# Performance work log

Measured on AMD Instinct MI355X. Metric: run time of the kernel, lower is better.

The kernel has to match this reference:

```python
import jax, jax.numpy as jnp
import numpy as np

B, T, D, K = 64, 512, 1024, 10
TEMP = 0.07
EPS = 1e-8


def setup_inputs() -> dict:
    key = jax.random.key(0)
    features = jax.random.normal(key, (B, T, D), dtype=jnp.float32)
    # Replicate torch.randperm-based negative sampling: for each batch b,
    # sample K indices without replacement from the (B-1)*T vectors of all
    # other batches, then map flat index -> (batch, time).
    rng = np.random.default_rng(0)
    neg_b = np.empty((B, K), dtype=np.int64)
    neg_t = np.empty((B, K), dtype=np.int64)
    for b in range(B):
        idx = rng.permutation((B - 1) * T)[:K]
        bb = idx // T
        bb = bb + (bb >= b)  # skip own batch
        neg_b[b] = bb
        neg_t[b] = idx % T
    return {"features": features, "neg_b": jnp.asarray(neg_b), "neg_t": jnp.asarray(neg_t)}


def _unit(x):
    # torch F.cosine_similarity semantics: divide by max(||x||, eps)
    n = jnp.sqrt(jnp.sum(x * x, axis=-1, keepdims=True))
    return x / jnp.maximum(n, EPS)


def reference(features, neg_b, neg_t):
    anchors = features[:, 1:T - 1, :]     # [B, T-2, D]
    positives = features[:, 2:T, :]       # [B, T-2, D]
    a_hat = _unit(anchors)
    pos_sim = jnp.sum(a_hat * _unit(positives), axis=-1) / TEMP          # [B, T-2]
    negs = jax.lax.stop_gradient(features)[neg_b, neg_t]                  # [B, K, D]
    sim_neg = jnp.einsum('btd,bkd->btk', a_hat, _unit(negs)) / TEMP       # [B, T-2, K]
    exp_pos = jnp.exp(pos_sim)
    exp_neg = jnp.exp(sim_neg).sum(axis=-1)
    loss = -jnp.log(exp_pos / (exp_pos + exp_neg))                        # [B, T-2]
    return loss.mean(axis=1).mean()
```

## Files before the change

kernel.cpp:

```cpp
#include <hip/hip_runtime.h>

typedef unsigned int uint;
typedef _Float16 f16x2 __attribute__((ext_vector_type(2)));

#define B_ 64
#define T_ 512
#define K_ 10
constexpr float TEMP_ = 0.07f;
constexpr float EPS_ = 1e-8f;
constexpr int F4ROW = 256;
constexpr int APW = 8;
constexpr int NBLK = 16;
constexpr int ROWU = 512;

__device__ __forceinline__ float dot4(float4 a, float4 b) {
    return a.x * b.x + a.y * b.y + a.z * b.z + a.w * b.w;
}
__device__ __forceinline__ f16x2 bc_(uint u){ return __builtin_bit_cast(f16x2, u); }
__device__ __forceinline__ f16x2 pkrtz(float a, float b){
    return __builtin_bit_cast(f16x2, __builtin_amdgcn_cvt_pkrtz(a, b));
}
__device__ __forceinline__ uint pkrtz_u(float a, float b){
    return __builtin_bit_cast(uint, __builtin_amdgcn_cvt_pkrtz(a, b));
}

template <int CTRL>
__device__ __forceinline__ float dpp_add(float x){
    int y = __builtin_amdgcn_update_dpp(0, __float_as_int(x), CTRL, 0xf, 0xf, false);
    return x + __int_as_float(y);
}
__device__ __forceinline__ float red6(float x){
    x = dpp_add<0x128>(x);
    x = dpp_add<0x124>(x);
    x = dpp_add<0x122>(x);
    x = dpp_add<0x121>(x);
    x = dpp_add<0x142>(x);
    x = dpp_add<0x143>(x);
    return x;
}
__device__ __forceinline__ float red64(float x){
    x = red6(x);
    return __shfl(x, 63, 64);
}

__global__ __launch_bounds__(64) void signcl_prep(
    const float* __restrict__ features,
    const int* __restrict__ neg_b,
    const int* __restrict__ neg_t,
    uint* __restrict__ negs_pk)
{
    const int blk = blockIdx.x;
    const int b = blk / K_, k = blk % K_;
    const int l = threadIdx.x;

    const int nb = neg_b[b * K_ + k];
    const int nt = neg_t[b * K_ + k];
    const float4* rp = reinterpret_cast<const float4*>(features)
                       + ((size_t)nb * T_ + nt) * F4ROW + l * 4;
    float4 v0 = rp[0], v1 = rp[1], v2 = rp[2], v3 = rp[3];
    float ss = dot4(v0, v0) + dot4(v1, v1) + dot4(v2, v2) + dot4(v3, v3);
    ss = red64(ss);
    const float inv = 1.f / fmaxf(sqrtf(ss), EPS_);

    uint4* out = reinterpret_cast<uint4*>(negs_pk + ((size_t)b * K_ + k) * ROWU);
    uint4 o;
    o.x = pkrtz_u(v0.x * inv, v0.y * inv);
    o.y = pkrtz_u(v0.z * inv, v0.w * inv);
    o.z = pkrtz_u(v1.x * inv, v1.y * inv);
    o.w = pkrtz_u(v1.z * inv, v1.w * inv);
    out[l] = o;
    o.x = pkrtz_u(v2.x * inv, v2.y * inv);
    o.y = pkrtz_u(v2.z * inv, v2.w * inv);
    o.z = pkrtz_u(v3.x * inv, v3.y * inv);
    o.w = pkrtz_u(v3.z * inv, v3.w * inv);
    out[64 + l] = o;
}

#define PACK8(F, X0, X1, X2, X3)                              \
    F##0 = pkrtz(X0.x, X0.y);                                 \
    F##1 = pkrtz(X0.z, X0.w);                                 \
    F##2 = pkrtz(X1.x, X1.y);                                 \
    F##3 = pkrtz(X1.z, X1.w);                                 \
    F##4 = pkrtz(X2.x, X2.y);                                 \
    F##5 = pkrtz(X2.z, X2.w);                                 \
    F##6 = pkrtz(X3.x, X3.y);                                 \
    F##7 = pkrtz(X3.z, X3.w);

__global__ __launch_bounds__(256, 2) void signcl_main(
    const float* __restrict__ features,
    const uint* __restrict__ negs_pk,
    float* __restrict__ partials)
{
    __shared__ uint s_negs[K_ * ROWU];
    __shared__ float s_part[4];

    const int tid = threadIdx.x;
    const int l = tid & 63, w = tid >> 6;
    const int bid = blockIdx.x;
    const int b = bid >> 4;
    const int c = bid & (NBLK - 1);

    {
        const uint4* gsrc = reinterpret_cast<const uint4*>(negs_pk + (size_t)b * K_ * ROWU);
        uint4* sdst = reinterpret_cast<uint4*>(s_negs);
#pragma unroll
        for (int j = 0; j < 5; ++j) sdst[tid + j * 256] = gsrc[tid + j * 256];
    }
    __syncthreads();

    const float4* fb = reinterpret_cast<const float4*>(features) + (size_t)b * T_ * F4ROW;
    const uint4* n4 = reinterpret_cast<const uint4*>(s_negs);
    const int ta = 1 + c * 32 + w * APW;

    const float4* rA = fb + (size_t)ta * F4ROW + l * 4;
    const float4* rB = fb + (size_t)min(ta + 1, T_ - 1) * F4ROW + l * 4;
    const float4* rC = fb + (size_t)min(ta + 2, T_ - 1) * F4ROW + l * 4;
    float4 A0 = rA[0], A1 = rA[1], A2 = rA[2], A3 = rA[3];
    float4 B0 = rB[0], B1 = rB[1], B2 = rB[2], B3 = rB[3];
    float4 C0 = rC[0], C1 = rC[1], C2 = rC[2], C3 = rC[3];

    f16x2 FA0, FA1, FA2, FA3, FA4, FA5, FA6, FA7;
    f16x2 FB0, FB1, FB2, FB3, FB4, FB5, FB6, FB7;
    PACK8(FA, A0, A1, A2, A3);
    float ssA = dot4(A0, A0) + dot4(A1, A1) + dot4(A2, A2) + dot4(A3, A3);
    float invA = 1.f / fmaxf(sqrtf(red6(ssA)), EPS_);

    const float invT = 1.f / TEMP_;
    float lsum = 0.f;

#pragma unroll
    for (int j = 0; j < APW / 2; ++j){
        const int u = ta + 2 * j;

        float4 P0, P1, P2, P3, Q0, Q1, Q2, Q3;
        if (j < APW / 2 - 1){
            const float4* rP = fb + (size_t)min(u + 3, T_ - 1) * F4ROW + l * 4;
            const float4* rQ = fb + (size_t)min(u + 4, T_ - 1) * F4ROW + l * 4;
            P0 = rP[0]; P1 = rP[1]; P2 = rP[2]; P3 = rP[3];
            Q0 = rQ[0]; Q1 = rQ[1]; Q2 = rQ[2]; Q3 = rQ[3];
        }

        PACK8(FB, B0, B1, B2, B3);

        float ndu[K_], ndv[K_];
#pragma unroll
        for (int k = 0; k < K_; ++k){
            uint4 u0 = n4[k * 128 + l];
            uint4 u1 = n4[k * 128 + 64 + l];
            float su = 0.f, sv = 0.f;
            f16x2 e;
            e = bc_(u0.x); su = __builtin_amdgcn_fdot2(FA0, e, su, false); sv = __builtin_amdgcn_fdot2(FB0, e, sv, false);
            e = bc_(u0.y); su = __builtin_amdgcn_fdot2(FA1, e, su, false); sv = __builtin_amdgcn_fdot2(FB1, e, sv, false);
            e = bc_(u0.z); su = __builtin_amdgcn_fdot2(FA2, e, su, false); sv = __builtin_amdgcn_fdot2(FB2, e, sv, false);
            e = bc_(u0.w); su = __builtin_amdgcn_fdot2(FA3, e, su, false); sv = __builtin_amdgcn_fdot2(FB3, e, sv, false);
            e = bc_(u1.x); su = __builtin_amdgcn_fdot2(FA4, e, su, false); sv = __builtin_amdgcn_fdot2(FB4, e, sv, false);
            e = bc_(u1.y); su = __builtin_amdgcn_fdot2(FA5, e, su, false); sv = __builtin_amdgcn_fdot2(FB5, e, sv, false);
            e = bc_(u1.z); su = __builtin_amdgcn_fdot2(FA6, e, su, false); sv = __builtin_amdgcn_fdot2(FB6, e, sv, false);
            e = bc_(u1.w); su = __builtin_amdgcn_fdot2(FA7, e, su, false); sv = __builtin_amdgcn_fdot2(FB7, e, sv, false);
            ndu[k] = su; ndv[k] = sv;
        }

        float ssB  = dot4(B0, B0) + dot4(B1, B1) + dot4(B2, B2) + dot4(B3, B3);
        float ssC  = dot4(C0, C0) + dot4(C1, C1) + dot4(C2, C2) + dot4(C3, C3);
        float dpAB = dot4(A0, B0) + dot4(A1, B1) + dot4(A2, B2) + dot4(A3, B3);
        float dpBC = dot4(B0, C0) + dot4(B1, C1) + dot4(B2, C2) + dot4(B3, C3);

#pragma unroll
        for (int k = 0; k < K_; ++k){ ndu[k] = red6(ndu[k]); ndv[k] = red6(ndv[k]); }
        ssB = red6(ssB); ssC = red6(ssC); dpAB = red6(dpAB); dpBC = red6(dpBC);
        const float invB = 1.f / fmaxf(sqrtf(ssB), EPS_);
        const float invC = 1.f / fmaxf(sqrtf(ssC), EPS_);

        if (u <= T_ - 2){
            float pos = dpAB * invA * invB * invT;
            float sc = invA * invT;
            float se = 0.f;
#pragma unroll
            for (int k = 0; k < K_; ++k) se += __expf(ndu[k] * sc);
            lsum += __logf(__expf(pos) + se) - pos;
        }
        if (u + 1 <= T_ - 2){
            float pos = dpBC * invB * invC * invT;
            float sc = invB * invT;
            float se = 0.f;
#pragma unroll
            for (int k = 0; k < K_; ++k) se += __expf(ndv[k] * sc);
            lsum += __logf(__expf(pos) + se) - pos;
        }

        if (j < APW / 2 - 1){
            PACK8(FA, C0, C1, C2, C3);
            A0 = C0; A1 = C1; A2 = C2; A3 = C3;
            B0 = P0; B1 = P1; B2 = P2; B3 = P3;
            C0 = Q0; C1 = Q1; C2 = Q2; C3 = Q3;
            invA = invC;
        }
    }

    if (l == 63) s_part[w] = lsum;
    __syncthreads();
    if (tid == 0) partials[bid] = s_part[0] + s_part[1] + s_part[2] + s_part[3];
}

__global__ __launch_bounds__(256) void signcl_reduce(
    const float* __restrict__ partials, float* __restrict__ out)
{
    __shared__ float s_w[4];
    const int tid = threadIdx.x;
    float s = 0.f;
    for (int idx = tid; idx < B_ * NBLK; idx += 256) s += partials[idx];
#pragma unroll
    for (int m = 32; m >= 1; m >>= 1) s += __shfl_xor(s, m, 64);
    const int w = tid >> 6, lane = tid & 63;
    if (lane == 0) s_w[w] = s;
    __syncthreads();
    if (tid == 0) {
        float t = s_w[0] + s_w[1] + s_w[2] + s_w[3];
        out[0] = t / (float)(B_ * (T_ - 2));
    }
}

extern "C" void kernel_launch(void* const* d_in, const int* in_sizes, int n_in,
                              void* d_out, int out_size, void* d_ws, size_t ws_size,
                              hipStream_t stream) {
    const float* features = (const float*)d_in[0];
    const int* neg_b = (const int*)d_in[1];
    const int* neg_t = (const int*)d_in[2];
    uint* negs_pk = (uint*)d_ws;
    float* partials = (float*)((char*)d_ws + (2u << 20));

    signcl_prep<<<B_ * K_, 64, 0, stream>>>(features, neg_b, neg_t, negs_pk);
    signcl_main<<<B_ * NBLK, 256, 0, stream>>>(features, negs_pk, partials);
    signcl_reduce<<<1, 256, 0, stream>>>(partials, (float*)d_out);
}
```

Measured before the change: 44.67 us.

## Split main kernel into one wavefront per anchor pair, drop LDS staging

Replaces the 256-thread blocks, each of which walked 8 anchors per wave with register rotation and staged the packed negatives in LDS, with a grid of 64-thread blocks. Each block handles a single pair of consecutive anchors and reads the negatives straight from global memory. The aim is far more parallelism and no block-level sync or LDS fill. In exchange, the neighbouring rows that the old rotation reused are now reloaded, and negatives are read from global/L2 by every block. The reduce kernel now sums 64*255 partials instead of 64*16.

```diff
diff --git a/kernel.cpp b/kernel.cpp
--- a/kernel.cpp
+++ b/kernel.cpp
@@ -9,8 +9,7 @@
 constexpr float TEMP_ = 0.07f;
 constexpr float EPS_ = 1e-8f;
 constexpr int F4ROW = 256;
-constexpr int APW = 8;
-constexpr int NBLK = 16;
+constexpr int NPAIR = 255;
 constexpr int ROWU = 512;
 
 __device__ __forceinline__ float dot4(float4 a, float4 b) {
@@ -86,120 +85,84 @@
     F##6 = pkrtz(X3.x, X3.y);                                 \
     F##7 = pkrtz(X3.z, X3.w);
 
-__global__ __launch_bounds__(256, 2) void signcl_main(
+__global__ __launch_bounds__(64, 4) void signcl_main(
     const float* __restrict__ features,
     const uint* __restrict__ negs_pk,
     float* __restrict__ partials)
 {
-    __shared__ uint s_negs[K_ * ROWU];
-    __shared__ float s_part[4];
-
-    const int tid = threadIdx.x;
-    const int l = tid & 63, w = tid >> 6;
-    const int bid = blockIdx.x;
-    const int b = bid >> 4;
-    const int c = bid & (NBLK - 1);
-
-    {
-        const uint4* gsrc = reinterpret_cast<const uint4*>(negs_pk + (size_t)b * K_ * ROWU);
-        uint4* sdst = reinterpret_cast<uint4*>(s_negs);
-#pragma unroll
-        for (int j = 0; j < 5; ++j) sdst[tid + j * 256] = gsrc[tid + j * 256];
-    }
-    __syncthreads();
+    const int l = threadIdx.x;
+    const int c = blockIdx.x;
+    const int b = blockIdx.y;
+    const int u = 1 + 2 * c;
 
     const float4* fb = reinterpret_cast<const float4*>(features) + (size_t)b * T_ * F4ROW;
-    const uint4* n4 = reinterpret_cast<const uint4*>(s_negs);
-    const int ta = 1 + c * 32 + w * APW;
-
-    const float4* rA = fb + (size_t)ta * F4ROW + l * 4;
-    const float4* rB = fb + (size_t)min(ta + 1, T_ - 1) * F4ROW + l * 4;
-    const float4* rC = fb + (size_t)min(ta + 2, T_ - 1) * F4ROW + l * 4;
+    const float4* rA = fb + (size_t)u * F4ROW + l * 4;
+    const float4* rB = rA + F4ROW;
+    const float4* rC = rB + F4ROW;
     float4 A0 = rA[0], A1 = rA[1], A2 = rA[2], A3 = rA[3];
     float4 B0 = rB[0], B1 = rB[1], B2 = rB[2], B3 = rB[3];
     float4 C0 = rC[0], C1 = rC[1], C2 = rC[2], C3 = rC[3];
 
+    const uint4* n4 = reinterpret_cast<const uint4*>(negs_pk + (size_t)b * K_ * ROWU);
+
     f16x2 FA0, FA1, FA2, FA3, FA4, FA5, FA6, FA7;
     f16x2 FB0, FB1, FB2, FB3, FB4, FB5, FB6, FB7;
     PACK8(FA, A0, A1, A2, A3);
-    float ssA = dot4(A0, A0) + dot4(A1, A1) + dot4(A2, A2) + dot4(A3, A3);
-    float invA = 1.f / fmaxf(sqrtf(red6(ssA)), EPS_);
+    PACK8(FB, B0, B1, B2, B3);
+
+    float ndu[K_], ndv[K_];
+#pragma unroll
+    for (int k = 0; k < K_; ++k){
+        uint4 u0 = n4[k * 128 + l];
+        uint4 u1 = n4[k * 128 + 64 + l];
+        float su = 0.f, sv = 0.f;
+        f16x2 e;
+        e = bc_(u0.x); su = __builtin_amdgcn_fdot2(FA0, e, su, false); sv = __builtin_amdgcn_fdot2(FB0, e, sv, false);
+        e = bc_(u0.y); su = __builtin_amdgcn_fdot2(FA1, e, su, false); sv = __builtin_amdgcn_fdot2(FB1, e, sv, false);
+        e = bc_(u0.z); su = __builtin_amdgcn_fdot2(FA2, e, su, false); sv = __builtin_amdgcn_fdot2(FB2, e, sv, false);
+        e = bc_(u0.w); su = __builtin_amdgcn_fdot2(FA3, e, su, false); sv = __builtin_amdgcn_fdot2(FB3, e, sv, false);
+        e = bc_(u1.x); su = __builtin_amdgcn_fdot2(FA4, e, su, false); sv = __builtin_amdgcn_fdot2(FB4, e, sv, false);
+        e = bc_(u1.y); su = __builtin_amdgcn_fdot2(FA5, e, su, false); sv = __builtin_amdgcn_fdot2(FB5, e, sv, false);
+        e = bc_(u1.z); su = __builtin_amdgcn_fdot2(FA6, e, su, false); sv = __builtin_amdgcn_fdot2(FB6, e, sv, false);
+        e = bc_(u1.w); su = __builtin_amdgcn_fdot2(FA7, e, su, false); sv = __builtin_amdgcn_fdot2(FB7, e, sv, false);
+        ndu[k] = su; ndv[k] = sv;
+    }
+
+    float ssA  = dot4(A0, A0) + dot4(A1, A1) + dot4(A2, A2) + dot4(A3, A3);
+    float ssB  = dot4(B0, B0) + dot4(B1, B1) + dot4(B2, B2) + dot4(B3, B3);
+    float ssC  = dot4(C0, C0) + dot4(C1, C1) + dot4(C2, C2) + dot4(C3, C3);
+    float dpAB = dot4(A0, B0) + dot4(A1, B1) + dot4(A2, B2) + dot4(A3, B3);
+    float dpBC = dot4(B0, C0) + dot4(B1, C1) + dot4(B2, C2) + dot4(B3, C3);
+
+#pragma unroll
+    for (int k = 0; k < K_; ++k){ ndu[k] = red6(ndu[k]); ndv[k] = red6(ndv[k]); }
+    ssA = red6(ssA); ssB = red6(ssB); ssC = red6(ssC);
+    dpAB = red6(dpAB); dpBC = red6(dpBC);
 
     const float invT = 1.f / TEMP_;
-    float lsum = 0.f;
+    const float invA = 1.f / fmaxf(sqrtf(ssA), EPS_);
+    const float invB = 1.f / fmaxf(sqrtf(ssB), EPS_);
+    const float invC = 1.f / fmaxf(sqrtf(ssC), EPS_);
 
+    float lsum;
+    {
+        float pos = dpAB * invA * invB * invT;
+        float sc = invA * invT;
+        float se = 0.f;
 #pragma unroll
-    for (int j = 0; j < APW / 2; ++j){
-        const int u = ta + 2 * j;
-
-        float4 P0, P1, P2, P3, Q0, Q1, Q2, Q3;
-        if (j < APW / 2 - 1){
-            const float4* rP = fb + (size_t)min(u + 3, T_ - 1) * F4ROW + l * 4;
-            const float4* rQ = fb + (size_t)min(u + 4, T_ - 1) * F4ROW + l * 4;
-            P0 = rP[0]; P1 = rP[1]; P2 = rP[2]; P3 = rP[3];
-            Q0 = rQ[0]; Q1 = rQ[1]; Q2 = rQ[2]; Q3 = rQ[3];
-        }
-
-        PACK8(FB, B0, B1, B2, B3);
-
-        float ndu[K_], ndv[K_];
+        for (int k = 0; k < K_; ++k) se += __expf(ndu[k] * sc);
+        lsum = __logf(__expf(pos) + se) - pos;
+    }
+    {
+        float pos = dpBC * invB * invC * invT;
+        float sc = invB * invT;
+        float se = 0.f;
 #pragma unroll
-        for (int k = 0; k < K_; ++k){
-            uint4 u0 = n4[k * 128 + l];
-            uint4 u1 = n4[k * 128 + 64 + l];
-            float su = 0.f, sv = 0.f;
-            f16x2 e;
-            e = bc_(u0.x); su = __builtin_amdgcn_fdot2(FA0, e, su, false); sv = __builtin_amdgcn_fdot2(FB0, e, sv, false);
-            e = bc_(u0.y); su = __builtin_amdgcn_fdot2(FA1, e, su, false); sv = __builtin_amdgcn_fdot2(FB1, e, sv, false);
-            e = bc_(u0.z); su = __builtin_amdgcn_fdot2(FA2, e, su, false); sv = __builtin_amdgcn_fdot2(FB2, e, sv, false);
-            e = bc_(u0.w); su = __builtin_amdgcn_fdot2(FA3, e, su, false); sv = __builtin_amdgcn_fdot2(FB3, e, sv, false);
-            e = bc_(u1.x); su = __builtin_amdgcn_fdot2(FA4, e, su, false); sv = __builtin_amdgcn_fdot2(FB4, e, sv, false);
-            e = bc_(u1.y); su = __builtin_amdgcn_fdot2(FA5, e, su, false); sv = __builtin_amdgcn_fdot2(FB5, e, sv, false);
-            e = bc_(u1.z); su = __builtin_amdgcn_fdot2(FA6, e, su, false); sv = __builtin_amdgcn_fdot2(FB6, e, sv, false);
-            e = bc_(u1.w); su = __builtin_amdgcn_fdot2(FA7, e, su, false); sv = __builtin_amdgcn_fdot2(FB7, e, sv, false);
-            ndu[k] = su; ndv[k] = sv;
-        }
-
-        float ssB  = dot4(B0, B0) + dot4(B1, B1) + dot4(B2, B2) + dot4(B3, B3);
-        float ssC  = dot4(C0, C0) + dot4(C1, C1) + dot4(C2, C2) + dot4(C3, C3);
-        float dpAB = dot4(A0, B0) + dot4(A1, B1) + dot4(A2, B2) + dot4(A3, B3);
-        float dpBC = dot4(B0, C0) + dot4(B1, C1) + dot4(B2, C2) + dot4(B3, C3);
-
-#pragma unroll
-        for (int k = 0; k < K_; ++k){ ndu[k] = red6(ndu[k]); ndv[k] = red6(ndv[k]); }
-        ssB = red6(ssB); ssC = red6(ssC); dpAB = red6(dpAB); dpBC = red6(dpBC);
-        const float invB = 1.f / fmaxf(sqrtf(ssB), EPS_);
-        const float invC = 1.f / fmaxf(sqrtf(ssC), EPS_);
-
-        if (u <= T_ - 2){
-            float pos = dpAB * invA * invB * invT;
-            float sc = invA * invT;
-            float se = 0.f;
-#pragma unroll
-            for (int k = 0; k < K_; ++k) se += __expf(ndu[k] * sc);
-            lsum += __logf(__expf(pos) + se) - pos;
-        }
-        if (u + 1 <= T_ - 2){
-            float pos = dpBC * invB * invC * invT;
-            float sc = invB * invT;
-            float se = 0.f;
-#pragma unroll
-            for (int k = 0; k < K_; ++k) se += __expf(ndv[k] * sc);
-            lsum += __logf(__expf(pos) + se) - pos;
-        }
-
-        if (j < APW / 2 - 1){
-            PACK8(FA, C0, C1, C2, C3);
-            A0 = C0; A1 = C1; A2 = C2; A3 = C3;
-            B0 = P0; B1 = P1; B2 = P2; B3 = P3;
-            C0 = Q0; C1 = Q1; C2 = Q2; C3 = Q3;
-            invA = invC;
-        }
+        for (int k = 0; k < K_; ++k) se += __expf(ndv[k] * sc);
+        lsum += __logf(__expf(pos) + se) - pos;
     }
 
-    if (l == 63) s_part[w] = lsum;
-    __syncthreads();
-    if (tid == 0) partials[bid] = s_part[0] + s_part[1] + s_part[2] + s_part[3];
+    if (l == 63) partials[b * NPAIR + c] = lsum;
 }
 
 __global__ __launch_bounds__(256) void signcl_reduce(
@@ -208,7 +171,7 @@
     __shared__ float s_w[4];
     const int tid = threadIdx.x;
     float s = 0.f;
-    for (int idx = tid; idx < B_ * NBLK; idx += 256) s += partials[idx];
+    for (int idx = tid; idx < B_ * NPAIR; idx += 256) s += partials[idx];
 #pragma unroll
     for (int m = 32; m >= 1; m >>= 1) s += __shfl_xor(s, m, 64);
     const int w = tid >> 6, lane = tid & 63;
@@ -230,6 +193,6 @@
     float* partials = (float*)((char*)d_ws + (2u << 20));
 
     signcl_prep<<<B_ * K_, 64, 0, stream>>>(features, neg_b, neg_t, negs_pk);
-    signcl_main<<<B_ * NBLK, 256, 0, stream>>>(features, negs_pk, partials);
+    signcl_main<<<dim3(NPAIR, B_), 64, 0, stream>>>(features, negs_pk, partials);
     signcl_reduce<<<1, 256, 0, stream>>>(partials, (float*)d_out);
 }
```

Result: slower. 66.83 us (+49.6%).
